# Optimization experiments

Hardware: AMD Instinct MI355X
Metric: run time of the kernel (lower is better)

## Reference

```python
import jax, jax.numpy as jnp
import numpy as np

N_NODES = 100000
N_EDGES = 1600000
IN_FEATS = 128
N_HIDDEN = 128
N_CLASSES = 47


def _glorot(key, shape):
    fan_in, fan_out = shape
    lim = jnp.sqrt(6.0 / (fan_in + fan_out))
    return jax.random.uniform(key, shape, jnp.float32, -lim, lim)


def setup_inputs() -> dict:
    key = jax.random.key(0)
    ks = jax.random.split(key, 12)
    x = jax.random.normal(ks[0], (N_NODES, IN_FEATS), jnp.float32)
    src = jax.random.randint(ks[1], (N_EDGES,), 0, N_NODES, jnp.int32)
    dst = jax.random.randint(ks[2], (N_EDGES,), 0, N_NODES, jnp.int32)
    dims = [(IN_FEATS, N_HIDDEN), (N_HIDDEN, N_HIDDEN), (N_HIDDEN, N_CLASSES)]
    params = {}
    for l, (di, do) in enumerate(dims):
        params[f"Ws{l}"] = _glorot(ks[3 + 3 * l], (di, do))
        params[f"Wn{l}"] = _glorot(ks[4 + 3 * l], (di, do))
        params[f"b{l}"] = jnp.zeros((do,), jnp.float32)
    return {"x": x, "src": src, "dst": dst, **params}


def _sage_layer(h, src, dst, Ws, Wn, b):
    # mean aggregation over incoming edges (irregular gather + segment-reduce)
    n = h.shape[0]
    msg = h[src]  # [E, F]
    agg = jax.ops.segment_sum(msg, dst, num_segments=n)
    deg = jax.ops.segment_sum(jnp.ones((src.shape[0],), h.dtype), dst, num_segments=n)
    agg = agg / jnp.maximum(deg, 1.0)[:, None]
    return h @ Ws + agg @ Wn + b


def reference(x, src, dst, Ws0, Wn0, b0, Ws1, Wn1, b1, Ws2, Wn2, b2):
    layers = [(Ws0, Wn0, b0), (Ws1, Wn1, b1), (Ws2, Wn2, b2)]
    h = x
    for l, (Ws, Wn, b) in enumerate(layers):
        h = _sage_layer(h, src, dst, Ws, Wn, b)
        if l != len(layers) - 1:
            h = jax.nn.relu(h)  # dropout is identity at inference
    return h
```

## Files before the change

### kernel.cpp

```cpp
#include <hip/hip_runtime.h>
#include <cstdint>
#include <cstddef>

static const int NN = 100000;
static const int NE = 1600000;
static const int F  = 128;
static const int BKT_SHIFT = 9;
static const int BNODES = 1 << BKT_SHIFT;
static const int NBKT = (NN + BNODES - 1) >> BKT_SHIFT;
static const int PKCAP = 16384;
static const int SRC_BITS = 17;
static const unsigned SRC_MASK = (1u << SRC_BITS) - 1u;

typedef __attribute__((ext_vector_type(8))) short short8;
typedef __attribute__((ext_vector_type(4))) float float4v;
typedef __attribute__((ext_vector_type(2))) float f32x2;

static __device__ __forceinline__ unsigned f2bf(float f){
    unsigned u = __builtin_bit_cast(unsigned, f);
    return (u + 0x7FFFu + ((u >> 16) & 1u)) >> 16;
}
static __device__ __forceinline__ float bf_lo(unsigned u){
    return __builtin_bit_cast(float, u << 16);
}
static __device__ __forceinline__ float bf_hi(unsigned u){
    return __builtin_bit_cast(float, u & 0xFFFF0000u);
}

__global__ __launch_bounds__(256) void bscatter_k(
        const int* __restrict__ src, const int* __restrict__ dst,
        int* __restrict__ bfill, unsigned* __restrict__ pk, int E){
    __shared__ int hist[NBKT];
    __shared__ int gbase[NBKT];
    const int t = threadIdx.x;
    for (int i = t; i < NBKT; i += 256) hist[i] = 0;
    __syncthreads();
    const int e0 = blockIdx.x * 2048;
    int s[8], d[8], b[8], r[8];
    #pragma unroll
    for (int j = 0; j < 8; ++j){
        int e = e0 + j*256 + t;
        if (e < E){
            s[j] = src[e]; d[j] = dst[e];
            b[j] = d[j] >> BKT_SHIFT;
            r[j] = atomicAdd(&hist[b[j]], 1);
        }
    }
    __syncthreads();
    for (int i = t; i < NBKT; i += 256){
        int h = hist[i];
        int base = 0;
        if (h) base = atomicAdd(&bfill[i], h);
        gbase[i] = i*PKCAP + base;
    }
    __syncthreads();
    #pragma unroll
    for (int j = 0; j < 8; ++j){
        int e = e0 + j*256 + t;
        if (e < E)
            pk[gbase[b[j]] + r[j]] =
                (unsigned)s[j] | ((unsigned)(d[j] & (BNODES-1)) << SRC_BITS);
    }
}

__global__ __launch_bounds__(1024) void sort_k(
        const unsigned* __restrict__ pk, const int* __restrict__ bfill,
        int* __restrict__ row_ptr, int* __restrict__ ssorted, int N){
    __shared__ int bs[256];
    __shared__ int hc[BNODES];
    __shared__ int of[BNODES];
    __shared__ int fi[BNODES];
    const int b = blockIdx.x;
    const int t = threadIdx.x;
    if (t < 256) bs[t] = (t < NBKT) ? bfill[t] : 0;
    if (t < BNODES){ hc[t] = 0; fi[t] = 0; }
    __syncthreads();
    for (int off = 1; off < 256; off <<= 1){
        int add = (t < 256 && t >= off) ? bs[t-off] : 0;
        __syncthreads();
        if (t < 256) bs[t] += add;
        __syncthreads();
    }
    const int cntb = bfill[b];
    const int rbeg = bs[b] - cntb;
    const unsigned* mypk = pk + (size_t)b * PKCAP;
    for (int i = t; i < cntb; i += 1024)
        atomicAdd(&hc[mypk[i] >> SRC_BITS], 1);
    __syncthreads();
    if (t < BNODES) of[t] = hc[t];
    __syncthreads();
    for (int off = 1; off < BNODES; off <<= 1){
        int add = (t < BNODES && t >= off) ? of[t-off] : 0;
        __syncthreads();
        if (t < BNODES) of[t] += add;
        __syncthreads();
    }
    if (t < BNODES){
        int excl = of[t] - hc[t];
        of[t] = excl;
        int node = (b << BKT_SHIFT) + t;
        if (node < N) row_ptr[node] = rbeg + excl;
    }
    if (b == 0 && t == 0) row_ptr[N] = NE;
    __syncthreads();
    for (int i = t; i < cntb; i += 1024){
        unsigned p = mypk[i];
        int dl = (int)(p >> SRC_BITS);
        int pos = rbeg + of[dl] + atomicAdd(&fi[dl], 1);
        ssorted[pos] = (int)(p & SRC_MASK);
    }
}


__global__ void xconv_k(const float* __restrict__ x, unsigned short* __restrict__ xb, int n8){
    int i = blockIdx.x*256 + threadIdx.x;
    if (i < n8){
        float4 v0 = ((const float4*)x)[i*2];
        float4 v1 = ((const float4*)x)[i*2+1];
        uint4 o;
        o.x = f2bf(v0.x) | (f2bf(v0.y) << 16);
        o.y = f2bf(v0.z) | (f2bf(v0.w) << 16);
        o.z = f2bf(v1.x) | (f2bf(v1.y) << 16);
        o.w = f2bf(v1.z) | (f2bf(v1.w) << 16);
        ((uint4*)xb)[i] = o;
    }
}

__global__ void prepw_all_k(const float* __restrict__ Ws0, const float* __restrict__ Wn0,
                            const float* __restrict__ Ws1, const float* __restrict__ Wn1,
                            const float* __restrict__ Ws2, const float* __restrict__ Wn2,
                            unsigned short* __restrict__ Wt0, unsigned short* __restrict__ Wt1,
                            unsigned short* __restrict__ Wt2){
    int i = blockIdx.x*256 + threadIdx.x;
    const float* Ws; const float* Wn; unsigned short* Wt; int D; int idx;
    if (i < 32768){       Ws=Ws0; Wn=Wn0; Wt=Wt0; D=128; idx=i; }
    else if (i < 65536){  Ws=Ws1; Wn=Wn1; Wt=Wt1; D=128; idx=i-32768; }
    else {                Ws=Ws2; Wn=Wn2; Wt=Wt2; D=47;  idx=i-65536; }
    int n = idx >> 7, k = idx & 127;
    float v = 0.f;
    if (n < D)        v = Ws[k*D + n];
    else if (n < 2*D) v = Wn[k*D + (n - D)];
    Wt[n*128 + k] = (unsigned short)f2bf(v);
}


__global__ __launch_bounds__(256) void gemm_mfma_k(
        const unsigned short* __restrict__ hb,
        const unsigned short* __restrict__ Wt,
        const float* __restrict__ bias,
        unsigned short* __restrict__ Y,
        unsigned short* __restrict__ Z,
        int M, int D, int Dpad, int two_pass){
    __shared__ char ldsA[128*256];
    const int t = threadIdx.x;
    const int lane = t & 63;
    const int w = t >> 6;
    const int wm = w >> 1, wn = w & 1;
    int bid = blockIdx.x;
    int bx, by;
    if (two_pass){
        bx = (bid >> 4)*8 + (bid & 7);
        by = (bid >> 3) & 1;
    } else { bx = bid; by = 0; }
    const int tile = bx * 128;
    if (tile >= M) return;
    const int cbase = by * 128;

    #pragma unroll
    for (int i = 0; i < 8; ++i){
        int chunkid = i*4 + w;
        int lin = chunkid*64 + lane;
        int row = lin >> 4;
        int cs  = lin & 15;
        int grow = tile + row; if (grow >= M) grow = M - 1;
        const char* src = (const char*)hb + (size_t)grow*256 + ((size_t)(cs ^ (row & 7)) << 4);
        __builtin_amdgcn_global_load_lds(
            (const __attribute__((address_space(1))) void*)src,
            (__attribute__((address_space(3))) void*)(ldsA + (size_t)chunkid*1024 + (size_t)lane*16),
            16, 0, 0);
    }

    short8 bfrag[4][4];
    {
        int ncol = cbase + wn*64;
        #pragma unroll
        for (int n = 0; n < 4; ++n){
            int wrow = ncol + n*16 + (lane & 15);
            const unsigned short* bp = Wt + (size_t)wrow*128 + ((lane >> 4) * 8);
            #pragma unroll
            for (int kk = 0; kk < 4; ++kk)
                bfrag[n][kk] = *(const short8*)(bp + kk*32);
        }
    }

    float4v acc[4][4];
    #pragma unroll
    for (int m = 0; m < 4; ++m)
        #pragma unroll
        for (int n = 0; n < 4; ++n)
            acc[m][n] = (float4v){0.f,0.f,0.f,0.f};

    __syncthreads();

    #pragma unroll
    for (int m = 0; m < 4; ++m){
        int r = wm*64 + m*16 + (lane & 15);
        #pragma unroll
        for (int kk = 0; kk < 4; ++kk){
            int c = kk*4 + (lane >> 4);
            short8 a = *(const short8*)(ldsA + (size_t)r*256 + ((size_t)(c ^ (r & 7)) << 4));
            #pragma unroll
            for (int n = 0; n < 4; ++n)
                acc[m][n] = __builtin_amdgcn_mfma_f32_16x16x32_bf16(a, bfrag[n][kk], acc[m][n], 0, 0, 0);
        }
    }

    #pragma unroll
    for (int m = 0; m < 4; ++m){
        #pragma unroll
        for (int n = 0; n < 4; ++n){
            int c = cbase + wn*64 + n*16 + (lane & 15);
            #pragma unroll
            for (int j = 0; j < 4; ++j){
                int r = tile + wm*64 + m*16 + (lane >> 4)*4 + j;
                if (r < M){
                    float v = acc[m][n][j];
                    if (c < D){
                        v += bias[c];
                        Y[(size_t)r*Dpad + c] = (unsigned short)f2bf(v);
                    } else if (c < 2*D){
                        Z[(size_t)r*Dpad + (c - D)] = (unsigned short)f2bf(v);
                    }
                }
            }
        }
    }
}


__global__ __launch_bounds__(256) void agg128_k(
        const unsigned short* __restrict__ Yb, const unsigned short* __restrict__ Zb,
        const int* __restrict__ row_ptr, const int* __restrict__ ssorted,
        unsigned short* __restrict__ hout, int N){
    const int lane = threadIdx.x & 63;
    const int q   = lane >> 4;
    const int sub = lane & 15;
    const int node = blockIdx.x*4 + (threadIdx.x >> 6);
    if (node >= N) return;
    const int beg = __builtin_amdgcn_readfirstlane(row_ptr[node]);
    const int end = __builtin_amdgcn_readfirstlane(row_ptr[node+1]);
    const float inv = 1.0f / fmaxf((float)(end - beg), 1.0f);
    const char* zc = (const char*)Zb;
    const unsigned boff = (unsigned)(sub*16);
    f32x2 a0={0.f,0.f}, a1={0.f,0.f}, a2={0.f,0.f}, a3={0.f,0.f};
    for (int e = beg; e < end; e += 32){
        int s[8];
        #pragma unroll
        for (int j = 0; j < 8; ++j){
            int ei = e + 4*j + q;
            int ec = ei < end ? ei : end - 1;
            s[j] = ssorted[ec];
        }
        uint4 u[8];
        #pragma unroll
        for (int j = 0; j < 8; ++j)
            u[j] = *(const uint4*)(zc + ((unsigned)s[j]*256u + boff));
        #pragma unroll
        for (int j = 0; j < 8; ++j){
            if (e + 4*j + q < end){
                a0 += (f32x2){ bf_lo(u[j].x), bf_hi(u[j].x) };
                a1 += (f32x2){ bf_lo(u[j].y), bf_hi(u[j].y) };
                a2 += (f32x2){ bf_lo(u[j].z), bf_hi(u[j].z) };
                a3 += (f32x2){ bf_lo(u[j].w), bf_hi(u[j].w) };
            }
        }
    }
    a0.x += __shfl_xor(a0.x,16,64); a0.x += __shfl_xor(a0.x,32,64);
    a0.y += __shfl_xor(a0.y,16,64); a0.y += __shfl_xor(a0.y,32,64);
    a1.x += __shfl_xor(a1.x,16,64); a1.x += __shfl_xor(a1.x,32,64);
    a1.y += __shfl_xor(a1.y,16,64); a1.y += __shfl_xor(a1.y,32,64);
    a2.x += __shfl_xor(a2.x,16,64); a2.x += __shfl_xor(a2.x,32,64);
    a2.y += __shfl_xor(a2.y,16,64); a2.y += __shfl_xor(a2.y,32,64);
    a3.x += __shfl_xor(a3.x,16,64); a3.x += __shfl_xor(a3.x,32,64);
    a3.y += __shfl_xor(a3.y,16,64); a3.y += __shfl_xor(a3.y,32,64);
    if (q == 0){
        uint4 yu = *(const uint4*)((const char*)Yb + (size_t)node*256 + sub*16);
        float r0 = fmaxf(bf_lo(yu.x) + a0.x*inv, 0.f);
        float r1 = fmaxf(bf_hi(yu.x) + a0.y*inv, 0.f);
        float r2 = fmaxf(bf_lo(yu.y) + a1.x*inv, 0.f);
        float r3 = fmaxf(bf_hi(yu.y) + a1.y*inv, 0.f);
        float r4 = fmaxf(bf_lo(yu.z) + a2.x*inv, 0.f);
        float r5 = fmaxf(bf_hi(yu.z) + a2.y*inv, 0.f);
        float r6 = fmaxf(bf_lo(yu.w) + a3.x*inv, 0.f);
        float r7 = fmaxf(bf_hi(yu.w) + a3.y*inv, 0.f);
        uint4 o;
        o.x = f2bf(r0) | (f2bf(r1) << 16);
        o.y = f2bf(r2) | (f2bf(r3) << 16);
        o.z = f2bf(r4) | (f2bf(r5) << 16);
        o.w = f2bf(r6) | (f2bf(r7) << 16);
        *(uint4*)((char*)hout + (size_t)node*256 + sub*16) = o;
    }
}

__global__ __launch_bounds__(256) void aggfin_k(
        const unsigned short* __restrict__ Yb, const unsigned short* __restrict__ Zb,
        const int* __restrict__ row_ptr, const int* __restrict__ ssorted,
        float* __restrict__ out, int N){
    const int lane = threadIdx.x & 63;
    const int slot = lane >> 3;
    const int sub  = lane & 7;
    const int node = blockIdx.x*4 + (threadIdx.x >> 6);
    if (node >= N) return;
    const int beg = __builtin_amdgcn_readfirstlane(row_ptr[node]);
    const int end = __builtin_amdgcn_readfirstlane(row_ptr[node+1]);
    const float inv = 1.0f / fmaxf((float)(end - beg), 1.0f);
    const char* zc = (const char*)Zb;
    const unsigned boff = (unsigned)(sub*16);
    f32x2 a0={0.f,0.f}, a1={0.f,0.f}, a2={0.f,0.f}, a3={0.f,0.f};
    for (int e = beg; e < end; e += 32){
        int s[4];
        #pragma unroll
        for (int j = 0; j < 4; ++j){
            int ei = e + 8*j + slot;
            int ec = ei < end ? ei : end - 1;
            s[j] = ssorted[ec];
        }
        uint4 u[4];
        #pragma unroll
        for (int j = 0; j < 4; ++j)
            u[j] = *(const uint4*)(zc + ((unsigned)s[j]*128u + boff));
        #pragma unroll
        for (int j = 0; j < 4; ++j){
            if (e + 8*j + slot < end){
                a0 += (f32x2){ bf_lo(u[j].x), bf_hi(u[j].x) };
                a1 += (f32x2){ bf_lo(u[j].y), bf_hi(u[j].y) };
                a2 += (f32x2){ bf_lo(u[j].z), bf_hi(u[j].z) };
                a3 += (f32x2){ bf_lo(u[j].w), bf_hi(u[j].w) };
            }
        }
    }
    a0.x += __shfl_xor(a0.x,8,64); a0.x += __shfl_xor(a0.x,16,64); a0.x += __shfl_xor(a0.x,32,64);
    a0.y += __shfl_xor(a0.y,8,64); a0.y += __shfl_xor(a0.y,16,64); a0.y += __shfl_xor(a0.y,32,64);
    a1.x += __shfl_xor(a1.x,8,64); a1.x += __shfl_xor(a1.x,16,64); a1.x += __shfl_xor(a1.x,32,64);
    a1.y += __shfl_xor(a1.y,8,64); a1.y += __shfl_xor(a1.y,16,64); a1.y += __shfl_xor(a1.y,32,64);
    a2.x += __shfl_xor(a2.x,8,64); a2.x += __shfl_xor(a2.x,16,64); a2.x += __shfl_xor(a2.x,32,64);
    a2.y += __shfl_xor(a2.y,8,64); a2.y += __shfl_xor(a2.y,16,64); a2.y += __shfl_xor(a2.y,32,64);
    a3.x += __shfl_xor(a3.x,8,64); a3.x += __shfl_xor(a3.x,16,64); a3.x += __shfl_xor(a3.x,32,64);
    a3.y += __shfl_xor(a3.y,8,64); a3.y += __shfl_xor(a3.y,16,64); a3.y += __shfl_xor(a3.y,32,64);
    if (slot == 0){
        uint4 yu = *(const uint4*)((const char*)Yb + (size_t)node*128 + sub*16);
        float v[8];
        v[0] = bf_lo(yu.x) + a0.x*inv;
        v[1] = bf_hi(yu.x) + a0.y*inv;
        v[2] = bf_lo(yu.y) + a1.x*inv;
        v[3] = bf_hi(yu.y) + a1.y*inv;
        v[4] = bf_lo(yu.z) + a2.x*inv;
        v[5] = bf_hi(yu.z) + a2.y*inv;
        v[6] = bf_lo(yu.w) + a3.x*inv;
        v[7] = bf_hi(yu.w) + a3.y*inv;
        int f = sub*8;
        size_t o = (size_t)node*47 + f;
        #pragma unroll
        for (int k = 0; k < 8; ++k)
            if (f + k < 47) out[o + k] = v[k];
    }
}


extern "C" void kernel_launch(void* const* d_in, const int* in_sizes, int n_in,
                              void* d_out, int out_size, void* d_ws, size_t ws_size,
                              hipStream_t stream){
    const float* x   = (const float*)d_in[0];
    const int*   src = (const int*)  d_in[1];
    const int*   dstv= (const int*)  d_in[2];
    const float* Ws0 = (const float*)d_in[3];
    const float* Wn0 = (const float*)d_in[4];
    const float* b0  = (const float*)d_in[5];
    const float* Ws1 = (const float*)d_in[6];
    const float* Wn1 = (const float*)d_in[7];
    const float* b1  = (const float*)d_in[8];
    const float* Ws2 = (const float*)d_in[9];
    const float* Wn2 = (const float*)d_in[10];
    const float* b2  = (const float*)d_in[11];
    float* out = (float*)d_out;
    const int N = NN, E = NE;

    char* w = (char*)d_ws;
    size_t off = 0;
    auto alloc = [&](size_t bytes)->char*{
        char* p = w + off; off += (bytes + 255) & ~(size_t)255; return p;
    };
    int*   bfill   = (int*)  alloc((size_t)NBKT*4);
    int*   row_ptr = (int*)  alloc((size_t)(NN+1)*4);
    int*   ssorted = (int*)  alloc((size_t)E*4);
    unsigned* pk   = (unsigned*)alloc((size_t)NBKT*PKCAP*4);
    unsigned short* xb  = (unsigned short*)alloc((size_t)NN*F*2);
    unsigned short* hA  = (unsigned short*)alloc((size_t)NN*F*2);
    unsigned short* hB  = (unsigned short*)alloc((size_t)NN*F*2);
    unsigned short* Yb  = (unsigned short*)alloc((size_t)NN*F*2);
    unsigned short* Zb  = (unsigned short*)alloc((size_t)NN*F*2);
    unsigned short* Wt0 = (unsigned short*)alloc((size_t)256*128*2);
    unsigned short* Wt1 = (unsigned short*)alloc((size_t)256*128*2);
    unsigned short* Wt2 = (unsigned short*)alloc((size_t)128*128*2);
    (void)ws_size; (void)n_in; (void)in_sizes; (void)out_size;

    const int GE = (E + 2047)/2048;

    hipMemsetAsync(bfill, 0, (size_t)NBKT*4, stream);
    bscatter_k<<<GE, 256, 0, stream>>>(src, dstv, bfill, pk, E);
    sort_k    <<<NBKT, 1024, 0, stream>>>(pk, bfill, row_ptr, ssorted, N);

    xconv_k<<<(N*F/8 + 255)/256, 256, 0, stream>>>(x, xb, N*F/8);
    prepw_all_k<<<320, 256, 0, stream>>>(Ws0, Wn0, Ws1, Wn1, Ws2, Wn2, Wt0, Wt1, Wt2);

    const int GM = (N + 127)/128;
    const int G2 = ((GM + 7)/8) * 16;
    const int GA = (N + 3)/4;

    gemm_mfma_k<<<G2, 256, 0, stream>>>(xb, Wt0, b0, Yb, Zb, N, 128, 128, 1);
    agg128_k   <<<GA, 256, 0, stream>>>(Yb, Zb, row_ptr, ssorted, hA, N);
    gemm_mfma_k<<<G2, 256, 0, stream>>>(hA, Wt1, b1, Yb, Zb, N, 128, 128, 1);
    agg128_k   <<<GA, 256, 0, stream>>>(Yb, Zb, row_ptr, ssorted, hB, N);
    gemm_mfma_k<<<GM, 256, 0, stream>>>(hB, Wt2, b2, Yb, Zb, N, 47, 64, 0);
    aggfin_k   <<<GA, 256, 0, stream>>>(Yb, Zb, row_ptr, ssorted, out, N);
}
```

Measured before the change: 366.8 us.

## Fuse preprocessing kernels and overlap CSR sort with first-layer GEMM

Merges edge bucket scatter, the x-to-bf16 conversion and the weight transpose into one launch, dispatched by block index. Runs the per-bucket CSR sort in the same launch as the first-layer GEMM, so the two independent jobs can overlap. Buckets shrink from 512 to 128 nodes, so the sort uses 256-thread blocks and a reduction-based prefix. This cuts launch count and serialization, at the cost of losing the earlier GEMM block swizzle for L2 locality and making the fused kernels heterogeneous in register and LDS use.

```diff
diff --git a/kernel.cpp b/kernel.cpp
--- a/kernel.cpp
+++ b/kernel.cpp
@@ -5,12 +5,16 @@
 static const int NN = 100000;
 static const int NE = 1600000;
 static const int F  = 128;
-static const int BKT_SHIFT = 9;
+static const int BKT_SHIFT = 7;
 static const int BNODES = 1 << BKT_SHIFT;
 static const int NBKT = (NN + BNODES - 1) >> BKT_SHIFT;
-static const int PKCAP = 16384;
+static const int PKCAP = 4096;
 static const int SRC_BITS = 17;
 static const unsigned SRC_MASK = (1u << SRC_BITS) - 1u;
+
+static const int GM = (NN + 127)/128;
+static const int XCONV_B = (NN*F/8)/256;
+static const int PREPW_B = 320;
 
 typedef __attribute__((ext_vector_type(8))) short short8;
 typedef __attribute__((ext_vector_type(4))) float float4v;
@@ -27,94 +31,52 @@
     return __builtin_bit_cast(float, u & 0xFFFF0000u);
 }
 
-__global__ __launch_bounds__(256) void bscatter_k(
+
+__global__ __launch_bounds__(256) void prep_fused_k(
         const int* __restrict__ src, const int* __restrict__ dst,
-        int* __restrict__ bfill, unsigned* __restrict__ pk, int E){
-    __shared__ int hist[NBKT];
-    __shared__ int gbase[NBKT];
+        int* __restrict__ bfill, unsigned* __restrict__ pk,
+        const float* __restrict__ x, unsigned short* __restrict__ xb,
+        const float* __restrict__ Ws0, const float* __restrict__ Wn0,
+        const float* __restrict__ Ws1, const float* __restrict__ Wn1,
+        const float* __restrict__ Ws2, const float* __restrict__ Wn2,
+        unsigned short* __restrict__ Wt0, unsigned short* __restrict__ Wt1,
+        unsigned short* __restrict__ Wt2){
+    __shared__ int sh[2*NBKT];
+    const int bid = blockIdx.x;
     const int t = threadIdx.x;
-    for (int i = t; i < NBKT; i += 256) hist[i] = 0;
-    __syncthreads();
-    const int e0 = blockIdx.x * 2048;
-    int s[8], d[8], b[8], r[8];
-    #pragma unroll
-    for (int j = 0; j < 8; ++j){
-        int e = e0 + j*256 + t;
-        if (e < E){
-            s[j] = src[e]; d[j] = dst[e];
-            b[j] = d[j] >> BKT_SHIFT;
-            r[j] = atomicAdd(&hist[b[j]], 1);
-        }
-    }
-    __syncthreads();
-    for (int i = t; i < NBKT; i += 256){
-        int h = hist[i];
-        int base = 0;
-        if (h) base = atomicAdd(&bfill[i], h);
-        gbase[i] = i*PKCAP + base;
-    }
-    __syncthreads();
-    #pragma unroll
-    for (int j = 0; j < 8; ++j){
-        int e = e0 + j*256 + t;
-        if (e < E)
-            pk[gbase[b[j]] + r[j]] =
-                (unsigned)s[j] | ((unsigned)(d[j] & (BNODES-1)) << SRC_BITS);
-    }
-}
-
-__global__ __launch_bounds__(1024) void sort_k(
-        const unsigned* __restrict__ pk, const int* __restrict__ bfill,
-        int* __restrict__ row_ptr, int* __restrict__ ssorted, int N){
-    __shared__ int bs[256];
-    __shared__ int hc[BNODES];
-    __shared__ int of[BNODES];
-    __shared__ int fi[BNODES];
-    const int b = blockIdx.x;
-    const int t = threadIdx.x;
-    if (t < 256) bs[t] = (t < NBKT) ? bfill[t] : 0;
-    if (t < BNODES){ hc[t] = 0; fi[t] = 0; }
-    __syncthreads();
-    for (int off = 1; off < 256; off <<= 1){
-        int add = (t < 256 && t >= off) ? bs[t-off] : 0;
-        __syncthreads();
-        if (t < 256) bs[t] += add;
-        __syncthreads();
-    }
-    const int cntb = bfill[b];
-    const int rbeg = bs[b] - cntb;
-    const unsigned* mypk = pk + (size_t)b * PKCAP;
-    for (int i = t; i < cntb; i += 1024)
-        atomicAdd(&hc[mypk[i] >> SRC_BITS], 1);
-    __syncthreads();
-    if (t < BNODES) of[t] = hc[t];
-    __syncthreads();
-    for (int off = 1; off < BNODES; off <<= 1){
-        int add = (t < BNODES && t >= off) ? of[t-off] : 0;
-        __syncthreads();
-        if (t < BNODES) of[t] += add;
-        __syncthreads();
-    }
-    if (t < BNODES){
-        int excl = of[t] - hc[t];
-        of[t] = excl;
-        int node = (b << BKT_SHIFT) + t;
-        if (node < N) row_ptr[node] = rbeg + excl;
-    }
-    if (b == 0 && t == 0) row_ptr[N] = NE;
-    __syncthreads();
-    for (int i = t; i < cntb; i += 1024){
-        unsigned p = mypk[i];
-        int dl = (int)(p >> SRC_BITS);
-        int pos = rbeg + of[dl] + atomicAdd(&fi[dl], 1);
-        ssorted[pos] = (int)(p & SRC_MASK);
-    }
-}
-
-
-__global__ void xconv_k(const float* __restrict__ x, unsigned short* __restrict__ xb, int n8){
-    int i = blockIdx.x*256 + threadIdx.x;
-    if (i < n8){
+    if (bid < NBKT){
+        int* hist  = sh;
+        int* gbase = sh + NBKT;
+        for (int i = t; i < NBKT; i += 256) hist[i] = 0;
+        __syncthreads();
+        const int e0 = bid * 2048;
+        int s[8], d[8], b[8], r[8];
+        #pragma unroll
+        for (int j = 0; j < 8; ++j){
+            int e = e0 + j*256 + t;
+            if (e < NE){
+                s[j] = src[e]; d[j] = dst[e];
+                b[j] = d[j] >> BKT_SHIFT;
+                r[j] = atomicAdd(&hist[b[j]], 1);
+            }
+        }
+        __syncthreads();
+        for (int i = t; i < NBKT; i += 256){
+            int h = hist[i];
+            int base = 0;
+            if (h) base = atomicAdd(&bfill[i], h);
+            gbase[i] = i*PKCAP + base;
+        }
+        __syncthreads();
+        #pragma unroll
+        for (int j = 0; j < 8; ++j){
+            int e = e0 + j*256 + t;
+            if (e < NE)
+                pk[gbase[b[j]] + r[j]] =
+                    (unsigned)s[j] | ((unsigned)(d[j] & (BNODES-1)) << SRC_BITS);
+        }
+    } else if (bid < NBKT + XCONV_B){
+        int i = (bid - NBKT)*256 + t;
         float4 v0 = ((const float4*)x)[i*2];
         float4 v1 = ((const float4*)x)[i*2+1];
         uint4 o;
@@ -123,118 +85,168 @@
         o.z = f2bf(v1.x) | (f2bf(v1.y) << 16);
         o.w = f2bf(v1.z) | (f2bf(v1.w) << 16);
         ((uint4*)xb)[i] = o;
-    }
-}
-
-__global__ void prepw_all_k(const float* __restrict__ Ws0, const float* __restrict__ Wn0,
-                            const float* __restrict__ Ws1, const float* __restrict__ Wn1,
-                            const float* __restrict__ Ws2, const float* __restrict__ Wn2,
-                            unsigned short* __restrict__ Wt0, unsigned short* __restrict__ Wt1,
-                            unsigned short* __restrict__ Wt2){
-    int i = blockIdx.x*256 + threadIdx.x;
-    const float* Ws; const float* Wn; unsigned short* Wt; int D; int idx;
-    if (i < 32768){       Ws=Ws0; Wn=Wn0; Wt=Wt0; D=128; idx=i; }
-    else if (i < 65536){  Ws=Ws1; Wn=Wn1; Wt=Wt1; D=128; idx=i-32768; }
-    else {                Ws=Ws2; Wn=Wn2; Wt=Wt2; D=47;  idx=i-65536; }
-    int n = idx >> 7, k = idx & 127;
-    float v = 0.f;
-    if (n < D)        v = Ws[k*D + n];
-    else if (n < 2*D) v = Wn[k*D + (n - D)];
-    Wt[n*128 + k] = (unsigned short)f2bf(v);
-}
-
+    } else {
+        int i = (bid - NBKT - XCONV_B)*256 + t;
+        const float* Ws; const float* Wn; unsigned short* Wt; int D; int idx;
+        if (i < 32768){       Ws=Ws0; Wn=Wn0; Wt=Wt0; D=128; idx=i; }
+        else if (i < 65536){  Ws=Ws1; Wn=Wn1; Wt=Wt1; D=128; idx=i-32768; }
+        else {                Ws=Ws2; Wn=Wn2; Wt=Wt2; D=47;  idx=i-65536; }
+        int n = idx >> 7, k = idx & 127;
+        float v = 0.f;
+        if (n < D)        v = Ws[k*D + n];
+        else if (n < 2*D) v = Wn[k*D + (n - D)];
+        Wt[n*128 + k] = (unsigned short)f2bf(v);
+    }
+}
+
+
+#define GEMM_BODY(ldsA, hb, Wt, bias, Y, Z, M, D, Dpad, tile, cbase)              \
+{                                                                                  \
+    const int t_ = threadIdx.x;                                                    \
+    const int lane = t_ & 63;                                                      \
+    const int w_ = t_ >> 6;                                                        \
+    const int wm = w_ >> 1, wn = w_ & 1;                                           \
+    _Pragma("unroll")                                                              \
+    for (int i = 0; i < 8; ++i){                                                   \
+        int chunkid = i*4 + w_;                                                    \
+        int lin = chunkid*64 + lane;                                               \
+        int row = lin >> 4;                                                        \
+        int cs  = lin & 15;                                                        \
+        int grow = tile + row; if (grow >= M) grow = M - 1;                        \
+        const char* src_ = (const char*)hb + (size_t)grow*256                      \
+                         + ((size_t)(cs ^ (row & 7)) << 4);                        \
+        __builtin_amdgcn_global_load_lds(                                          \
+            (const __attribute__((address_space(1))) void*)src_,                   \
+            (__attribute__((address_space(3))) void*)(ldsA + (size_t)chunkid*1024  \
+                + (size_t)lane*16), 16, 0, 0);                                     \
+    }                                                                              \
+    short8 bfrag[4][4];                                                            \
+    {                                                                              \
+        int ncol = cbase + wn*64;                                                  \
+        _Pragma("unroll")                                                          \
+        for (int n = 0; n < 4; ++n){                                               \
+            int wrow = ncol + n*16 + (lane & 15);                                  \
+            const unsigned short* bp = Wt + (size_t)wrow*128 + ((lane >> 4) * 8);  \
+            _Pragma("unroll")                                                      \
+            for (int kk = 0; kk < 4; ++kk)                                         \
+                bfrag[n][kk] = *(const short8*)(bp + kk*32);                       \
+        }                                                                          \
+    }                                                                              \
+    float4v acc[4][4];                                                             \
+    _Pragma("unroll")                                                              \
+    for (int m = 0; m < 4; ++m)                                                    \
+        _Pragma("unroll")                                                          \
+        for (int n = 0; n < 4; ++n)                                                \
+            acc[m][n] = (float4v){0.f,0.f,0.f,0.f};                                \
+    __syncthreads();                                                               \
+    _Pragma("unroll")                                                              \
+    for (int m = 0; m < 4; ++m){                                                   \
+        int r = wm*64 + m*16 + (lane & 15);                                        \
+        _Pragma("unroll")                                                          \
+        for (int kk = 0; kk < 4; ++kk){                                            \
+            int c = kk*4 + (lane >> 4);                                            \
+            short8 a = *(const short8*)(ldsA + (size_t)r*256                       \
+                      + ((size_t)(c ^ (r & 7)) << 4));                             \
+            _Pragma("unroll")                                                      \
+            for (int n = 0; n < 4; ++n)                                            \
+                acc[m][n] = __builtin_amdgcn_mfma_f32_16x16x32_bf16(               \
+                                a, bfrag[n][kk], acc[m][n], 0, 0, 0);              \
+        }                                                                          \
+    }                                                                              \
+    _Pragma("unroll")                                                              \
+    for (int m = 0; m < 4; ++m){                                                   \
+        _Pragma("unroll")                                                          \
+        for (int n = 0; n < 4; ++n){                                               \
+            int c = cbase + wn*64 + n*16 + (lane & 15);                            \
+            _Pragma("unroll")                                                      \
+            for (int j = 0; j < 4; ++j){                                           \
+                int r = tile + wm*64 + m*16 + (lane >> 4)*4 + j;                   \
+                if (r < M){                                                        \
+                    float v = acc[m][n][j];                                        \
+                    if (c < D){                                                    \
+                        v += bias[c];                                              \
+                        Y[(size_t)r*Dpad + c] = (unsigned short)f2bf(v);           \
+                    } else if (c < 2*D){                                           \
+                        Z[(size_t)r*Dpad + (c - D)] = (unsigned short)f2bf(v);     \
+                    }                                                              \
+                }                                                                  \
+            }                                                                      \
+        }                                                                          \
+    }                                                                              \
+}
+
+
+__global__ __launch_bounds__(256) void sort_gemm_k(
+        const unsigned* __restrict__ pk, const int* __restrict__ bfill,
+        int* __restrict__ row_ptr, int* __restrict__ ssorted,
+        const unsigned short* __restrict__ hb, const unsigned short* __restrict__ Wt,
+        const float* __restrict__ bias,
+        unsigned short* __restrict__ Y, unsigned short* __restrict__ Z, int N){
+    __shared__ char smem[128*256];
+    const int bid = blockIdx.x;
+    const int t = threadIdx.x;
+    if (bid < NBKT){
+        int* hc  = (int*)smem;
+        int* of  = hc + 128;
+        int* fi  = of + 128;
+        int* red = fi + 128;
+        const int b = bid;
+        int part = 0;
+        for (int i = t; i < b; i += 256) part += bfill[i];
+        red[t] = part;
+        if (t < 128){ hc[t] = 0; fi[t] = 0; }
+        __syncthreads();
+        for (int off = 128; off > 0; off >>= 1){
+            if (t < off) red[t] += red[t+off];
+            __syncthreads();
+        }
+        const int rbeg = red[0];
+        const int cntb = bfill[b];
+        const unsigned* mypk = pk + (size_t)b * PKCAP;
+        for (int i = t; i < cntb; i += 256)
+            atomicAdd(&hc[mypk[i] >> SRC_BITS], 1);
+        __syncthreads();
+        if (t < 128) of[t] = hc[t];
+        __syncthreads();
+        for (int off = 1; off < 128; off <<= 1){
+            int add = (t < 128 && t >= off) ? of[t-off] : 0;
+            __syncthreads();
+            if (t < 128) of[t] += add;
+            __syncthreads();
+        }
+        if (t < 128){
+            int excl = of[t] - hc[t];
+            of[t] = excl;
+            int node = (b << BKT_SHIFT) + t;
+            if (node < N) row_ptr[node] = rbeg + excl;
+        }
+        if (b == 0 && t == 0) row_ptr[N] = NE;
+        __syncthreads();
+        for (int i = t; i < cntb; i += 256){
+            unsigned p = mypk[i];
+            int dl = (int)(p >> SRC_BITS);
+            int pos = rbeg + of[dl] + atomicAdd(&fi[dl], 1);
+            ssorted[pos] = (int)(p & SRC_MASK);
+        }
+    } else {
+        int bid2 = bid - NBKT;
+        int bx = bid2 % GM;
+        int by = bid2 / GM;
+        const int tile = bx * 128;
+        const int cbase = by * 128;
+        GEMM_BODY(smem, hb, Wt, bias, Y, Z, N, 128, 128, tile, cbase)
+    }
+}
 
 __global__ __launch_bounds__(256) void gemm_mfma_k(
-        const unsigned short* __restrict__ hb,
-        const unsigned short* __restrict__ Wt,
+        const unsigned short* __restrict__ hb, const unsigned short* __restrict__ Wt,
         const float* __restrict__ bias,
-        unsigned short* __restrict__ Y,
-        unsigned short* __restrict__ Z,
-        int M, int D, int Dpad, int two_pass){
+        unsigned short* __restrict__ Y, unsigned short* __restrict__ Z,
+        int M, int D, int Dpad){
     __shared__ char ldsA[128*256];
-    const int t = threadIdx.x;
-    const int lane = t & 63;
-    const int w = t >> 6;
-    const int wm = w >> 1, wn = w & 1;
-    int bid = blockIdx.x;
-    int bx, by;
-    if (two_pass){
-        bx = (bid >> 4)*8 + (bid & 7);
-        by = (bid >> 3) & 1;
-    } else { bx = bid; by = 0; }
-    const int tile = bx * 128;
-    if (tile >= M) return;
-    const int cbase = by * 128;
-
-    #pragma unroll
-    for (int i = 0; i < 8; ++i){
-        int chunkid = i*4 + w;
-        int lin = chunkid*64 + lane;
-        int row = lin >> 4;
-        int cs  = lin & 15;
-        int grow = tile + row; if (grow >= M) grow = M - 1;
-        const char* src = (const char*)hb + (size_t)grow*256 + ((size_t)(cs ^ (row & 7)) << 4);
-        __builtin_amdgcn_global_load_lds(
-            (const __attribute__((address_space(1))) void*)src,
-            (__attribute__((address_space(3))) void*)(ldsA + (size_t)chunkid*1024 + (size_t)lane*16),
-            16, 0, 0);
-    }
-
-    short8 bfrag[4][4];
-    {
-        int ncol = cbase + wn*64;
-        #pragma unroll
-        for (int n = 0; n < 4; ++n){
-            int wrow = ncol + n*16 + (lane & 15);
-            const unsigned short* bp = Wt + (size_t)wrow*128 + ((lane >> 4) * 8);
-            #pragma unroll
-            for (int kk = 0; kk < 4; ++kk)
-                bfrag[n][kk] = *(const short8*)(bp + kk*32);
-        }
-    }
-
-    float4v acc[4][4];
-    #pragma unroll
-    for (int m = 0; m < 4; ++m)
-        #pragma unroll
-        for (int n = 0; n < 4; ++n)
-            acc[m][n] = (float4v){0.f,0.f,0.f,0.f};
-
-    __syncthreads();
-
-    #pragma unroll
-    for (int m = 0; m < 4; ++m){
-        int r = wm*64 + m*16 + (lane & 15);
-        #pragma unroll
-        for (int kk = 0; kk < 4; ++kk){
-            int c = kk*4 + (lane >> 4);
-            short8 a = *(const short8*)(ldsA + (size_t)r*256 + ((size_t)(c ^ (r & 7)) << 4));
-            #pragma unroll
-            for (int n = 0; n < 4; ++n)
-                acc[m][n] = __builtin_amdgcn_mfma_f32_16x16x32_bf16(a, bfrag[n][kk], acc[m][n], 0, 0, 0);
-        }
-    }
-
-    #pragma unroll
-    for (int m = 0; m < 4; ++m){
-        #pragma unroll
-        for (int n = 0; n < 4; ++n){
-            int c = cbase + wn*64 + n*16 + (lane & 15);
-            #pragma unroll
-            for (int j = 0; j < 4; ++j){
-                int r = tile + wm*64 + m*16 + (lane >> 4)*4 + j;
-                if (r < M){
-                    float v = acc[m][n][j];
-                    if (c < D){
-                        v += bias[c];
-                        Y[(size_t)r*Dpad + c] = (unsigned short)f2bf(v);
-                    } else if (c < 2*D){
-                        Z[(size_t)r*Dpad + (c - D)] = (unsigned short)f2bf(v);
-                    }
-                }
-            }
-        }
-    }
+    const int tile = blockIdx.x * 128;
+    const int cbase = blockIdx.y * 128;
+    GEMM_BODY(ldsA, hb, Wt, bias, Y, Z, M, D, Dpad, tile, cbase)
 }
 
 
@@ -383,7 +395,7 @@
     const float* Wn2 = (const float*)d_in[10];
     const float* b2  = (const float*)d_in[11];
     float* out = (float*)d_out;
-    const int N = NN, E = NE;
+    const int N = NN;
 
     char* w = (char*)d_ws;
     size_t off = 0;
@@ -392,7 +404,7 @@
     };
     int*   bfill   = (int*)  alloc((size_t)NBKT*4);
     int*   row_ptr = (int*)  alloc((size_t)(NN+1)*4);
-    int*   ssorted = (int*)  alloc((size_t)E*4);
+    int*   ssorted = (int*)  alloc((size_t)NE*4);
     unsigned* pk   = (unsigned*)alloc((size_t)NBKT*PKCAP*4);
     unsigned short* xb  = (unsigned short*)alloc((size_t)NN*F*2);
     unsigned short* hA  = (unsigned short*)alloc((size_t)NN*F*2);
@@ -404,23 +416,20 @@
     unsigned short* Wt2 = (unsigned short*)alloc((size_t)128*128*2);
     (void)ws_size; (void)n_in; (void)in_sizes; (void)out_size;
 
-    const int GE = (E + 2047)/2048;
-
     hipMemsetAsync(bfill, 0, (size_t)NBKT*4, stream);
-    bscatter_k<<<GE, 256, 0, stream>>>(src, dstv, bfill, pk, E);
-    sort_k    <<<NBKT, 1024, 0, stream>>>(pk, bfill, row_ptr, ssorted, N);
-
-    xconv_k<<<(N*F/8 + 255)/256, 256, 0, stream>>>(x, xb, N*F/8);
-    prepw_all_k<<<320, 256, 0, stream>>>(Ws0, Wn0, Ws1, Wn1, Ws2, Wn2, Wt0, Wt1, Wt2);
-
-    const int GM = (N + 127)/128;
-    const int G2 = ((GM + 7)/8) * 16;
+
+    prep_fused_k<<<NBKT + XCONV_B + PREPW_B, 256, 0, stream>>>(
+        src, dstv, bfill, pk, x, xb,
+        Ws0, Wn0, Ws1, Wn1, Ws2, Wn2, Wt0, Wt1, Wt2);
+
+    sort_gemm_k<<<NBKT + 2*GM, 256, 0, stream>>>(
+        pk, bfill, row_ptr, ssorted, xb, Wt0, b0, Yb, Zb, N);
+
     const int GA = (N + 3)/4;
 
-    gemm_mfma_k<<<G2, 256, 0, stream>>>(xb, Wt0, b0, Yb, Zb, N, 128, 128, 1);
     agg128_k   <<<GA, 256, 0, stream>>>(Yb, Zb, row_ptr, ssorted, hA, N);
-    gemm_mfma_k<<<G2, 256, 0, stream>>>(hA, Wt1, b1, Yb, Zb, N, 128, 128, 1);
+    gemm_mfma_k<<<dim3(GM,2), 256, 0, stream>>>(hA, Wt1, b1, Yb, Zb, N, 128, 128);
     agg128_k   <<<GA, 256, 0, stream>>>(Yb, Zb, row_ptr, ssorted, hB, N);
-    gemm_mfma_k<<<GM, 256, 0, stream>>>(hB, Wt2, b2, Yb, Zb, N, 47, 64, 0);
+    gemm_mfma_k<<<dim3(GM,1), 256, 0, stream>>>(hB, Wt2, b2, Yb, Zb, N, 47, 64);
     aggfin_k   <<<GA, 256, 0, stream>>>(Yb, Zb, row_ptr, ssorted, out, N);
 }
```

Result: faster. 351.4 us (-4.2%).

## Fuse preprocessing kernels and co-schedule CSR sort with first GEMM

Applied to the files above, without the earlier changes.

Merges the edge bucket scatter, x-to-bf16 conversion and weight transpose into one launch. It then runs the per-bucket CSR sort alongside the layer-0 GEMM in a single grid, which works because the two are independent. Buckets shrink from 512 to 128 nodes, so each sort block does less work and the prefix over buckets becomes a block reduction. The 128-wide GEMMs now use 512-thread blocks covering all 256 output columns, replacing the two-pass column split. The goal is fewer launches and more overlap of small serial stages, at the cost of less uniform blocks and a smaller per-bucket capacity (4096) that could overflow on skewed degree distributions.

```diff
diff --git a/kernel.cpp b/kernel.cpp
--- a/kernel.cpp
+++ b/kernel.cpp
@@ -5,12 +5,16 @@
 static const int NN = 100000;
 static const int NE = 1600000;
 static const int F  = 128;
-static const int BKT_SHIFT = 9;
+static const int BKT_SHIFT = 7;
 static const int BNODES = 1 << BKT_SHIFT;
 static const int NBKT = (NN + BNODES - 1) >> BKT_SHIFT;
-static const int PKCAP = 16384;
+static const int PKCAP = 4096;
 static const int SRC_BITS = 17;
 static const unsigned SRC_MASK = (1u << SRC_BITS) - 1u;
+
+static const int GM = (NN + 127)/128;
+static const int XCONV_B = (NN*F/8)/256;
+static const int PREPW_B = 320;
 
 typedef __attribute__((ext_vector_type(8))) short short8;
 typedef __attribute__((ext_vector_type(4))) float float4v;
@@ -27,94 +31,52 @@
     return __builtin_bit_cast(float, u & 0xFFFF0000u);
 }
 
-__global__ __launch_bounds__(256) void bscatter_k(
+
+__global__ __launch_bounds__(256) void prep_fused_k(
         const int* __restrict__ src, const int* __restrict__ dst,
-        int* __restrict__ bfill, unsigned* __restrict__ pk, int E){
-    __shared__ int hist[NBKT];
-    __shared__ int gbase[NBKT];
+        int* __restrict__ bfill, unsigned* __restrict__ pk,
+        const float* __restrict__ x, unsigned short* __restrict__ xb,
+        const float* __restrict__ Ws0, const float* __restrict__ Wn0,
+        const float* __restrict__ Ws1, const float* __restrict__ Wn1,
+        const float* __restrict__ Ws2, const float* __restrict__ Wn2,
+        unsigned short* __restrict__ Wt0, unsigned short* __restrict__ Wt1,
+        unsigned short* __restrict__ Wt2){
+    __shared__ int sh[2*NBKT];
+    const int bid = blockIdx.x;
     const int t = threadIdx.x;
-    for (int i = t; i < NBKT; i += 256) hist[i] = 0;
-    __syncthreads();
-    const int e0 = blockIdx.x * 2048;
-    int s[8], d[8], b[8], r[8];
-    #pragma unroll
-    for (int j = 0; j < 8; ++j){
-        int e = e0 + j*256 + t;
-        if (e < E){
-            s[j] = src[e]; d[j] = dst[e];
-            b[j] = d[j] >> BKT_SHIFT;
-            r[j] = atomicAdd(&hist[b[j]], 1);
-        }
-    }
-    __syncthreads();
-    for (int i = t; i < NBKT; i += 256){
-        int h = hist[i];
-        int base = 0;
-        if (h) base = atomicAdd(&bfill[i], h);
-        gbase[i] = i*PKCAP + base;
-    }
-    __syncthreads();
-    #pragma unroll
-    for (int j = 0; j < 8; ++j){
-        int e = e0 + j*256 + t;
-        if (e < E)
-            pk[gbase[b[j]] + r[j]] =
-                (unsigned)s[j] | ((unsigned)(d[j] & (BNODES-1)) << SRC_BITS);
-    }
-}
-
-__global__ __launch_bounds__(1024) void sort_k(
-        const unsigned* __restrict__ pk, const int* __restrict__ bfill,
-        int* __restrict__ row_ptr, int* __restrict__ ssorted, int N){
-    __shared__ int bs[256];
-    __shared__ int hc[BNODES];
-    __shared__ int of[BNODES];
-    __shared__ int fi[BNODES];
-    const int b = blockIdx.x;
-    const int t = threadIdx.x;
-    if (t < 256) bs[t] = (t < NBKT) ? bfill[t] : 0;
-    if (t < BNODES){ hc[t] = 0; fi[t] = 0; }
-    __syncthreads();
-    for (int off = 1; off < 256; off <<= 1){
-        int add = (t < 256 && t >= off) ? bs[t-off] : 0;
-        __syncthreads();
-        if (t < 256) bs[t] += add;
-        __syncthreads();
-    }
-    const int cntb = bfill[b];
-    const int rbeg = bs[b] - cntb;
-    const unsigned* mypk = pk + (size_t)b * PKCAP;
-    for (int i = t; i < cntb; i += 1024)
-        atomicAdd(&hc[mypk[i] >> SRC_BITS], 1);
-    __syncthreads();
-    if (t < BNODES) of[t] = hc[t];
-    __syncthreads();
-    for (int off = 1; off < BNODES; off <<= 1){
-        int add = (t < BNODES && t >= off) ? of[t-off] : 0;
-        __syncthreads();
-        if (t < BNODES) of[t] += add;
-        __syncthreads();
-    }
-    if (t < BNODES){
-        int excl = of[t] - hc[t];
-        of[t] = excl;
-        int node = (b << BKT_SHIFT) + t;
-        if (node < N) row_ptr[node] = rbeg + excl;
-    }
-    if (b == 0 && t == 0) row_ptr[N] = NE;
-    __syncthreads();
-    for (int i = t; i < cntb; i += 1024){
-        unsigned p = mypk[i];
-        int dl = (int)(p >> SRC_BITS);
-        int pos = rbeg + of[dl] + atomicAdd(&fi[dl], 1);
-        ssorted[pos] = (int)(p & SRC_MASK);
-    }
-}
-
-
-__global__ void xconv_k(const float* __restrict__ x, unsigned short* __restrict__ xb, int n8){
-    int i = blockIdx.x*256 + threadIdx.x;
-    if (i < n8){
+    if (bid < NBKT){
+        int* hist  = sh;
+        int* gbase = sh + NBKT;
+        for (int i = t; i < NBKT; i += 256) hist[i] = 0;
+        __syncthreads();
+        const int e0 = bid * 2048;
+        int s[8], d[8], b[8], r[8];
+        #pragma unroll
+        for (int j = 0; j < 8; ++j){
+            int e = e0 + j*256 + t;
+            if (e < NE){
+                s[j] = src[e]; d[j] = dst[e];
+                b[j] = d[j] >> BKT_SHIFT;
+                r[j] = atomicAdd(&hist[b[j]], 1);
+            }
+        }
+        __syncthreads();
+        for (int i = t; i < NBKT; i += 256){
+            int h = hist[i];
+            int base = 0;
+            if (h) base = atomicAdd(&bfill[i], h);
+            gbase[i] = i*PKCAP + base;
+        }
+        __syncthreads();
+        #pragma unroll
+        for (int j = 0; j < 8; ++j){
+            int e = e0 + j*256 + t;
+            if (e < NE)
+                pk[gbase[b[j]] + r[j]] =
+                    (unsigned)s[j] | ((unsigned)(d[j] & (BNODES-1)) << SRC_BITS);
+        }
+    } else if (bid < NBKT + XCONV_B){
+        int i = (bid - NBKT)*256 + t;
         float4 v0 = ((const float4*)x)[i*2];
         float4 v1 = ((const float4*)x)[i*2+1];
         uint4 o;
@@ -123,52 +85,35 @@
         o.z = f2bf(v1.x) | (f2bf(v1.y) << 16);
         o.w = f2bf(v1.z) | (f2bf(v1.w) << 16);
         ((uint4*)xb)[i] = o;
-    }
-}
-
-__global__ void prepw_all_k(const float* __restrict__ Ws0, const float* __restrict__ Wn0,
-                            const float* __restrict__ Ws1, const float* __restrict__ Wn1,
-                            const float* __restrict__ Ws2, const float* __restrict__ Wn2,
-                            unsigned short* __restrict__ Wt0, unsigned short* __restrict__ Wt1,
-                            unsigned short* __restrict__ Wt2){
-    int i = blockIdx.x*256 + threadIdx.x;
-    const float* Ws; const float* Wn; unsigned short* Wt; int D; int idx;
-    if (i < 32768){       Ws=Ws0; Wn=Wn0; Wt=Wt0; D=128; idx=i; }
-    else if (i < 65536){  Ws=Ws1; Wn=Wn1; Wt=Wt1; D=128; idx=i-32768; }
-    else {                Ws=Ws2; Wn=Wn2; Wt=Wt2; D=47;  idx=i-65536; }
-    int n = idx >> 7, k = idx & 127;
-    float v = 0.f;
-    if (n < D)        v = Ws[k*D + n];
-    else if (n < 2*D) v = Wn[k*D + (n - D)];
-    Wt[n*128 + k] = (unsigned short)f2bf(v);
-}
-
-
-__global__ __launch_bounds__(256) void gemm_mfma_k(
-        const unsigned short* __restrict__ hb,
-        const unsigned short* __restrict__ Wt,
+    } else {
+        int i = (bid - NBKT - XCONV_B)*256 + t;
+        const float* Ws; const float* Wn; unsigned short* Wt; int D; int idx;
+        if (i < 32768){       Ws=Ws0; Wn=Wn0; Wt=Wt0; D=128; idx=i; }
+        else if (i < 65536){  Ws=Ws1; Wn=Wn1; Wt=Wt1; D=128; idx=i-32768; }
+        else {                Ws=Ws2; Wn=Wn2; Wt=Wt2; D=47;  idx=i-65536; }
+        int n = idx >> 7, k = idx & 127;
+        float v = 0.f;
+        if (n < D)        v = Ws[k*D + n];
+        else if (n < 2*D) v = Wn[k*D + (n - D)];
+        Wt[n*128 + k] = (unsigned short)f2bf(v);
+    }
+}
+
+
+template<int WAVES, int WN>
+static __device__ __forceinline__ void gemm_body(char* ldsA,
+        const unsigned short* __restrict__ hb, const unsigned short* __restrict__ Wt,
         const float* __restrict__ bias,
-        unsigned short* __restrict__ Y,
-        unsigned short* __restrict__ Z,
-        int M, int D, int Dpad, int two_pass){
-    __shared__ char ldsA[128*256];
+        unsigned short* __restrict__ Y, unsigned short* __restrict__ Z,
+        int M, int D, int Dpad, int tile, int cbase){
     const int t = threadIdx.x;
     const int lane = t & 63;
     const int w = t >> 6;
-    const int wm = w >> 1, wn = w & 1;
-    int bid = blockIdx.x;
-    int bx, by;
-    if (two_pass){
-        bx = (bid >> 4)*8 + (bid & 7);
-        by = (bid >> 3) & 1;
-    } else { bx = bid; by = 0; }
-    const int tile = bx * 128;
-    if (tile >= M) return;
-    const int cbase = by * 128;
+    const int wm = w / WN, wn = w % WN;
 
     #pragma unroll
-    for (int i = 0; i < 8; ++i){
-        int chunkid = i*4 + w;
+    for (int i = 0; i < 32/WAVES; ++i){
+        int chunkid = i*WAVES + w;
         int lin = chunkid*64 + lane;
         int row = lin >> 4;
         int cs  = lin & 15;
@@ -235,6 +180,83 @@
             }
         }
     }
+}
+
+
+__global__ __launch_bounds__(512) void sort_gemm_k(
+        const unsigned* __restrict__ pk, const int* __restrict__ bfill,
+        int* __restrict__ row_ptr, int* __restrict__ ssorted,
+        const unsigned short* __restrict__ hb, const unsigned short* __restrict__ Wt,
+        const float* __restrict__ bias,
+        unsigned short* __restrict__ Y, unsigned short* __restrict__ Z, int N){
+    __shared__ char smem[128*256];
+    const int bid = blockIdx.x;
+    const int t = threadIdx.x;
+    if (bid < NBKT){
+        int* hc  = (int*)smem;
+        int* of  = hc + 128;
+        int* fi  = of + 128;
+        int* red = fi + 128;
+        const int b = bid;
+        int part = 0;
+        for (int i = t; i < b; i += 512) part += bfill[i];
+        red[t] = part;
+        if (t < 128){ hc[t] = 0; fi[t] = 0; }
+        __syncthreads();
+        for (int off = 256; off > 0; off >>= 1){
+            if (t < off) red[t] += red[t+off];
+            __syncthreads();
+        }
+        const int rbeg = red[0];
+        const int cntb = bfill[b];
+        const unsigned* mypk = pk + (size_t)b * PKCAP;
+        for (int i = t; i < cntb; i += 512)
+            atomicAdd(&hc[mypk[i] >> SRC_BITS], 1);
+        __syncthreads();
+        if (t < 128) of[t] = hc[t];
+        __syncthreads();
+        for (int off = 1; off < 128; off <<= 1){
+            int add = (t < 128 && t >= off) ? of[t-off] : 0;
+            __syncthreads();
+            if (t < 128) of[t] += add;
+            __syncthreads();
+        }
+        if (t < 128){
+            int excl = of[t] - hc[t];
+            of[t] = excl;
+            int node = (b << BKT_SHIFT) + t;
+            if (node < N) row_ptr[node] = rbeg + excl;
+        }
+        if (b == 0 && t == 0) row_ptr[N] = NE;
+        __syncthreads();
+        for (int i = t; i < cntb; i += 512){
+            unsigned p = mypk[i];
+            int dl = (int)(p >> SRC_BITS);
+            int pos = rbeg + of[dl] + atomicAdd(&fi[dl], 1);
+            ssorted[pos] = (int)(p & SRC_MASK);
+        }
+    } else {
+        const int tile = (bid - NBKT) * 128;
+        gemm_body<8,4>(smem, hb, Wt, bias, Y, Z, N, 128, 128, tile, 0);
+    }
+}
+
+__global__ __launch_bounds__(512) void gemm512_k(
+        const unsigned short* __restrict__ hb, const unsigned short* __restrict__ Wt,
+        const float* __restrict__ bias,
+        unsigned short* __restrict__ Y, unsigned short* __restrict__ Z,
+        int M, int D, int Dpad){
+    __shared__ char ldsA[128*256];
+    gemm_body<8,4>(ldsA, hb, Wt, bias, Y, Z, M, D, Dpad, blockIdx.x*128, 0);
+}
+
+__global__ __launch_bounds__(256) void gemm256_k(
+        const unsigned short* __restrict__ hb, const unsigned short* __restrict__ Wt,
+        const float* __restrict__ bias,
+        unsigned short* __restrict__ Y, unsigned short* __restrict__ Z,
+        int M, int D, int Dpad){
+    __shared__ char ldsA[128*256];
+    gemm_body<4,2>(ldsA, hb, Wt, bias, Y, Z, M, D, Dpad, blockIdx.x*128, 0);
 }
 
 
@@ -383,7 +405,7 @@
     const float* Wn2 = (const float*)d_in[10];
     const float* b2  = (const float*)d_in[11];
     float* out = (float*)d_out;
-    const int N = NN, E = NE;
+    const int N = NN;
 
     char* w = (char*)d_ws;
     size_t off = 0;
@@ -392,7 +414,7 @@
     };
     int*   bfill   = (int*)  alloc((size_t)NBKT*4);
     int*   row_ptr = (int*)  alloc((size_t)(NN+1)*4);
-    int*   ssorted = (int*)  alloc((size_t)E*4);
+    int*   ssorted = (int*)  alloc((size_t)NE*4);
     unsigned* pk   = (unsigned*)alloc((size_t)NBKT*PKCAP*4);
     unsigned short* xb  = (unsigned short*)alloc((size_t)NN*F*2);
     unsigned short* hA  = (unsigned short*)alloc((size_t)NN*F*2);
@@ -404,23 +426,20 @@
     unsigned short* Wt2 = (unsigned short*)alloc((size_t)128*128*2);
     (void)ws_size; (void)n_in; (void)in_sizes; (void)out_size;
 
-    const int GE = (E + 2047)/2048;
-
     hipMemsetAsync(bfill, 0, (size_t)NBKT*4, stream);
-    bscatter_k<<<GE, 256, 0, stream>>>(src, dstv, bfill, pk, E);
-    sort_k    <<<NBKT, 1024, 0, stream>>>(pk, bfill, row_ptr, ssorted, N);
-
-    xconv_k<<<(N*F/8 + 255)/256, 256, 0, stream>>>(x, xb, N*F/8);
-    prepw_all_k<<<320, 256, 0, stream>>>(Ws0, Wn0, Ws1, Wn1, Ws2, Wn2, Wt0, Wt1, Wt2);
-
-    const int GM = (N + 127)/128;
-    const int G2 = ((GM + 7)/8) * 16;
+
+    prep_fused_k<<<NBKT + XCONV_B + PREPW_B, 256, 0, stream>>>(
+        src, dstv, bfill, pk, x, xb,
+        Ws0, Wn0, Ws1, Wn1, Ws2, Wn2, Wt0, Wt1, Wt2);
+
+    sort_gemm_k<<<NBKT + GM, 512, 0, stream>>>(
+        pk, bfill, row_ptr, ssorted, xb, Wt0, b0, Yb, Zb, N);
+
     const int GA = (N + 3)/4;
 
-    gemm_mfma_k<<<G2, 256, 0, stream>>>(xb, Wt0, b0, Yb, Zb, N, 128, 128, 1);
-    agg128_k   <<<GA, 256, 0, stream>>>(Yb, Zb, row_ptr, ssorted, hA, N);
-    gemm_mfma_k<<<G2, 256, 0, stream>>>(hA, Wt1, b1, Yb, Zb, N, 128, 128, 1);
-    agg128_k   <<<GA, 256, 0, stream>>>(Yb, Zb, row_ptr, ssorted, hB, N);
-    gemm_mfma_k<<<GM, 256, 0, stream>>>(hB, Wt2, b2, Yb, Zb, N, 47, 64, 0);
-    aggfin_k   <<<GA, 256, 0, stream>>>(Yb, Zb, row_ptr, ssorted, out, N);
-}
+    agg128_k <<<GA, 256, 0, stream>>>(Yb, Zb, row_ptr, ssorted, hA, N);
+    gemm512_k<<<GM, 512, 0, stream>>>(hA, Wt1, b1, Yb, Zb, N, 128, 128);
+    agg128_k <<<GA, 256, 0, stream>>>(Yb, Zb, row_ptr, ssorted, hB, N);
+    gemm256_k<<<GM, 256, 0, stream>>>(hB, Wt2, b2, Yb, Zb, N, 47, 64);
+    aggfin_k <<<GA, 256, 0, stream>>>(Yb, Zb, row_ptr, ssorted, out, N);
+}
```

After: 343.3 us. 1.07x faster.
